# Kernel optimization log

Hardware: AMD Instinct MI355X
Metric: run time of the kernel (lower is better)

Reference implementation:

```python
import jax, jax.numpy as jnp
import numpy as np

N_NODES = 100000
N_EDGES = 1600000
D_FEAT = 128
HIDDEN = 64
N_CLASSES = 40
NEG_SLOPE = 0.01  # jax.nn.leaky_relu default, matches flax nn.leaky_relu


def glorot(key, shape):
    fan_in, fan_out = shape
    return jax.random.normal(key, shape, dtype=jnp.float32) * jnp.sqrt(2.0 / (fan_in + fan_out))


def setup_inputs() -> dict:
    key = jax.random.key(0)
    ks = jax.random.split(key, 8)
    nodes = jax.random.normal(ks[0], (N_NODES, D_FEAT), dtype=jnp.float32)
    senders = jax.random.randint(ks[1], (N_EDGES,), 0, N_NODES, dtype=jnp.int32)
    receivers = jax.random.randint(ks[2], (N_EDGES,), 0, N_NODES, dtype=jnp.int32)
    W1 = glorot(ks[3], (D_FEAT, HIDDEN))
    b1 = jnp.zeros((HIDDEN,), jnp.float32)
    W2 = glorot(ks[4], (HIDDEN, HIDDEN))
    b2 = jnp.zeros((HIDDEN,), jnp.float32)
    W3 = glorot(ks[5], (HIDDEN, N_CLASSES))
    b3 = jnp.zeros((N_CLASSES,), jnp.float32)
    return {"nodes": nodes, "senders": senders, "receivers": receivers,
            "W1": W1, "b1": b1, "W2": W2, "b2": b2, "W3": W3, "b3": b3}


def gcn_aggregate(x, senders, receivers, n_nodes):
    """jraph.GraphConvolution symmetric_normalization aggregation (post update_node_fn)."""
    ones = jnp.ones(senders.shape[0], dtype=x.dtype)
    sender_deg = jax.ops.segment_sum(ones, senders, num_segments=n_nodes)
    receiver_deg = jax.ops.segment_sum(ones, receivers, num_segments=n_nodes)
    x = x * jax.lax.rsqrt(jnp.maximum(sender_deg, 1.0))[:, None]
    x = jax.ops.segment_sum(x[senders], receivers, num_segments=n_nodes)  # [N, F]
    x = x * jax.lax.rsqrt(jnp.maximum(receiver_deg, 1.0))[:, None]
    return x


def reference(nodes, senders, receivers, W1, b1, W2, b2, W3, b3):
    n = nodes.shape[0]
    # Layer 1: GraphConvolution(MLP([hidden, hidden], leaky_relu))
    h = jax.nn.leaky_relu(nodes @ W1 + b1, NEG_SLOPE)
    h = jax.nn.leaky_relu(h @ W2 + b2, NEG_SLOPE)
    h = gcn_aggregate(h, senders, receivers, n)
    # Dropout is deterministic (training=False) -> identity
    # Layer 2: GraphConvolution(Dense(number_classes))
    h = h @ W3 + b3
    h = gcn_aggregate(h, senders, receivers, n)
    return jax.nn.softmax(h, axis=-1)
```

## Files before the change

kernel.cpp:

```cpp
#include <hip/hip_runtime.h>
#include <hip/hip_fp16.h>

#define NEG_SLOPE 0.01f
#define RANGE_BITS 15
#define RANGE (1 << RANGE_BITS)
#define HWORDS (RANGE / 2)
#define SLICE_BITS 16
#define SLICE (1 << SLICE_BITS)
#define PSTRIDE 64

typedef _Float16 f16x8 __attribute__((ext_vector_type(8)));
typedef float f32x4 __attribute__((ext_vector_type(4)));

__device__ __forceinline__ float lrelu(float x) { return x > 0.f ? x : NEG_SLOPE * x; }

__device__ __forceinline__ unsigned pack2h(float a, float b) {
    __half2 h = __floats2half2_rn(a, b);
    unsigned u; __builtin_memcpy(&u, &h, 4); return u;
}
__device__ __forceinline__ float2 unpack2(unsigned u) {
    __half2 h = *reinterpret_cast<__half2*>(&u);
    return __half22float2(h);
}
__device__ __forceinline__ f16x8 u4h8(uint4 u) {
    f16x8 r; __builtin_memcpy(&r, &u, 16); return r;
}

__global__ __launch_bounds__(1024) void count_kernel(
    const int* __restrict__ snd, const int* __restrict__ rcv,
    unsigned* __restrict__ partial, unsigned short* __restrict__ pos16,
    int nE, int NR, int NS)
{
    __shared__ unsigned hist[HWORDS];
    const int b = blockIdx.x;
    const int a = b / (NR * NS);
    const int rem = b - a * NR * NS;
    const int r = rem / NS;
    const int s = rem - r * NS;
    const int t = threadIdx.x;
    for (int k = t; k < HWORDS; k += 1024) hist[k] = 0u;
    __syncthreads();
    const int base = r << RANGE_BITS;
    const int lo = s << SLICE_BITS;
    const int hi = min(lo + SLICE, nE);
    const int n4 = (hi - lo) >> 2;
    const int* arr = (a == 0) ? rcv : snd;
    const int4* arr4 = (const int4*)(arr + lo);
    if (a == 0) {
        for (int i4 = t; i4 < n4; i4 += 1024) {
            const int4 v = arr4[i4];
            const int ib = lo + i4 * 4;
            int vv[4] = {v.x, v.y, v.z, v.w};
#pragma unroll
            for (int c = 0; c < 4; ++c) {
                const unsigned d = (unsigned)(vv[c] - base);
                if (d < (unsigned)RANGE) {
                    const unsigned sh = (d & 1u) << 4;
                    const unsigned old = atomicAdd(&hist[d >> 1], 1u << sh);
                    pos16[ib + c] = (unsigned short)((old >> sh) & 0xffffu);
                }
            }
        }
        for (int i = lo + n4 * 4 + t; i < hi; i += 1024) {
            const unsigned d = (unsigned)(arr[i] - base);
            if (d < (unsigned)RANGE) {
                const unsigned sh = (d & 1u) << 4;
                const unsigned old = atomicAdd(&hist[d >> 1], 1u << sh);
                pos16[i] = (unsigned short)((old >> sh) & 0xffffu);
            }
        }
    } else {
        for (int i4 = t; i4 < n4; i4 += 1024) {
            const int4 v = arr4[i4];
            int vv[4] = {v.x, v.y, v.z, v.w};
#pragma unroll
            for (int c = 0; c < 4; ++c) {
                const unsigned d = (unsigned)(vv[c] - base);
                if (d < (unsigned)RANGE) atomicAdd(&hist[d >> 1], 1u << ((d & 1u) << 4));
            }
        }
        for (int i = lo + n4 * 4 + t; i < hi; i += 1024) {
            const unsigned d = (unsigned)(arr[i] - base);
            if (d < (unsigned)RANGE) atomicAdd(&hist[d >> 1], 1u << ((d & 1u) << 4));
        }
    }
    __syncthreads();
    unsigned* dst = partial + (size_t)((a * NR + r) * NS + s) * HWORDS;
    for (int k = t; k < HWORDS; k += 1024) dst[k] = hist[k];
}

__global__ __launch_bounds__(256) void scanp_kernel(
    unsigned* __restrict__ partial,
    int* __restrict__ dr_i,
    float* __restrict__ rin, float* __restrict__ rout,
    int nN, int NR, int NS)
{
    const int gid = blockIdx.x * 256 + threadIdx.x;
    if (gid >= NR * HWORDS) return;
    const int r  = gid >> (RANGE_BITS - 1);
    const int wd = gid & (HWORDS - 1);
    unsigned* prcv = partial + (size_t)(r * NS) * HWORDS + wd;
    unsigned run0 = 0, run1 = 0;
    for (int s = 0; s < NS; ++s) {
        unsigned* p = prcv + (size_t)s * HWORDS;
        const unsigned c = *p;
        *p = run0 | (run1 << 16);
        run0 += c & 0xffffu;
        run1 += c >> 16;
    }
    const unsigned* psnd = partial + (size_t)((NR + r) * NS) * HWORDS + wd;
    unsigned t0 = 0, t1 = 0;
    for (int s = 0; s < NS; ++s) {
        const unsigned c = psnd[(size_t)s * HWORDS];
        t0 += c & 0xffffu;
        t1 += c >> 16;
    }
    const int n0 = (r << RANGE_BITS) + 2 * wd;
    if (n0 < nN) {
        dr_i[n0] = (int)run0;
        rout[n0] = rsqrtf(fmaxf((float)run0, 1.f));
        rin[n0]  = rsqrtf(fmaxf((float)t0, 1.f));
    }
    if (n0 + 1 < nN) {
        dr_i[n0 + 1] = (int)run1;
        rout[n0 + 1] = rsqrtf(fmaxf((float)run1, 1.f));
        rin[n0 + 1]  = rsqrtf(fmaxf((float)t1, 1.f));
    }
}

__global__ __launch_bounds__(256) void scan1_kernel(const int* __restrict__ cnt,
                                                    int* __restrict__ rowptr,
                                                    int* __restrict__ bsums, int n)
{
    __shared__ int sd[256];
    const int t = threadIdx.x;
    const int base = blockIdx.x * 1024 + t * 4;
    int v0 = (base + 0 < n) ? cnt[base + 0] : 0;
    int v1 = (base + 1 < n) ? cnt[base + 1] : 0;
    int v2 = (base + 2 < n) ? cnt[base + 2] : 0;
    int v3 = (base + 3 < n) ? cnt[base + 3] : 0;
    const int p1 = v0, p2 = v0 + v1, p3 = v0 + v1 + v2;
    const int tot = p3 + v3;
    sd[t] = tot;
    __syncthreads();
    for (int off = 1; off < 256; off <<= 1) {
        int y = (t >= off) ? sd[t - off] : 0;
        __syncthreads();
        sd[t] += y;
        __syncthreads();
    }
    const int excl = sd[t] - tot;
    if (base + 0 < n) rowptr[base + 0] = excl;
    if (base + 1 < n) rowptr[base + 1] = excl + p1;
    if (base + 2 < n) rowptr[base + 2] = excl + p2;
    if (base + 3 < n) rowptr[base + 3] = excl + p3;
    if (t == 255) bsums[blockIdx.x] = sd[255];
}

__global__ __launch_bounds__(256) void scan2_kernel(int* __restrict__ bsums, int nb)
{
    __shared__ int sd[256];
    const int t = threadIdx.x;
    const int v = (t < nb) ? bsums[t] : 0;
    sd[t] = v;
    __syncthreads();
    for (int off = 1; off < 256; off <<= 1) {
        int y = (t >= off) ? sd[t - off] : 0;
        __syncthreads();
        sd[t] += y;
        __syncthreads();
    }
    if (t < nb) bsums[t] = sd[t] - v;
}

__global__ __launch_bounds__(256) void scan3_kernel(int* __restrict__ rowptr,
                                                    const int* __restrict__ bsums,
                                                    int n, int nE)
{
    const int gid = blockIdx.x * 256 + threadIdx.x;
    if (gid < n) rowptr[gid] += bsums[gid >> 10];
    if (gid == 0) rowptr[n] = nE;
}

__global__ __launch_bounds__(256) void fillmlp_kernel(
    const float* __restrict__ X, const float* __restrict__ W1, const float* __restrict__ b1,
    const float* __restrict__ W2, const float* __restrict__ b2, const float* __restrict__ W3,
    const float* __restrict__ rin, __half* __restrict__ p, int nN, int NB_MLP,
    const int* __restrict__ snd, const int* __restrict__ rcv,
    const unsigned short* __restrict__ pos16, const unsigned* __restrict__ partial,
    const int* __restrict__ rowptr, int* __restrict__ csr_src, int nE, int NS)
{
    __shared__ uint4 R1[1024];
    __shared__ uint4 R2[512];

    const int blk = (int)blockIdx.x;
    if (blk < NB_MLP) {
        const int t    = threadIdx.x;
        const int w    = t >> 6;
        const int l    = t & 63;
        const int lrow = l & 15;
        const int lq   = l >> 4;
        const int row0 = blk * 64;

        {
            const int c = l;
            for (int ch = 0; ch < 4; ++ch) {
                const int kc = 4 * w + ch;
                const float* wp = W1 + (kc * 8) * 64 + c;
                uint4 u;
                u.x = pack2h(wp[0],       wp[64]);
                u.y = pack2h(wp[2 * 64],  wp[3 * 64]);
                u.z = pack2h(wp[4 * 64],  wp[5 * 64]);
                u.w = pack2h(wp[6 * 64],  wp[7 * 64]);
                R1[c * 16 + (kc ^ (c & 7))] = u;
            }
        }

        const int grow = row0 + 16 * w + lrow;
        const bool rowok = grow < nN;
        const float* xr = X + (size_t)grow * 128 + lq * 8;

        float4 xa[4], xb[4];
#pragma unroll
        for (int ks = 0; ks < 4; ++ks) {
            xa[ks] = make_float4(0.f, 0.f, 0.f, 0.f);
            xb[ks] = xa[ks];
            if (rowok) {
                xa[ks] = *(const float4*)(xr + 32 * ks);
                xb[ks] = *(const float4*)(xr + 32 * ks + 4);
            }
        }
        __syncthreads();

        f32x4 acc1[4];
#pragma unroll
        for (int nt = 0; nt < 4; ++nt) acc1[nt] = (f32x4){0.f, 0.f, 0.f, 0.f};

#pragma unroll
        for (int ks = 0; ks < 4; ++ks) {
            uint4 au;
            au.x = pack2h(xa[ks].x, xa[ks].y); au.y = pack2h(xa[ks].z, xa[ks].w);
            au.z = pack2h(xb[ks].x, xb[ks].y); au.w = pack2h(xb[ks].z, xb[ks].w);
            const f16x8 af = u4h8(au);
            const int kc = 4 * ks + lq;
#pragma unroll
            for (int nt = 0; nt < 4; ++nt) {
                const int c = 16 * nt + lrow;
                const uint4 bu = R1[c * 16 + (kc ^ (c & 7))];
                acc1[nt] = __builtin_amdgcn_mfma_f32_16x16x32_f16(af, u4h8(bu), acc1[nt], 0, 0, 0);
            }
        }
        __syncthreads();

        {
            __half* hh = (__half*)R2;
#pragma unroll
            for (int nt = 0; nt < 4; ++nt) {
                const int col = 16 * nt + lrow;
                const float bv = b1[col];
                const int ch = col >> 3, cl = col & 7;
#pragma unroll
                for (int r = 0; r < 4; ++r) {
                    const int rw = 16 * w + 4 * lq + r;
                    hh[rw * 64 + ((ch ^ (rw & 7)) * 8) + cl] = __float2half(lrelu(acc1[nt][r] + bv));
                }
            }
            const int c = l;
#pragma unroll
            for (int ch = 0; ch < 2; ++ch) {
                const int kc = 2 * w + ch;
                const float* wp = W2 + (kc * 8) * 64 + c;
                uint4 u;
                u.x = pack2h(wp[0],      wp[64]);
                u.y = pack2h(wp[2 * 64], wp[3 * 64]);
                u.z = pack2h(wp[4 * 64], wp[5 * 64]);
                u.w = pack2h(wp[6 * 64], wp[7 * 64]);
                R1[c * 8 + (kc ^ (c & 7))] = u;
            }
            if (c < 48) {
                const bool cv = c < 40;
#pragma unroll
                for (int ch = 0; ch < 2; ++ch) {
                    const int kc = 2 * w + ch;
                    const float* wp = W3 + (kc * 8) * 40 + c;
                    uint4 u;
                    u.x = pack2h(cv ? wp[0]      : 0.f, cv ? wp[40]     : 0.f);
                    u.y = pack2h(cv ? wp[2 * 40] : 0.f, cv ? wp[3 * 40] : 0.f);
                    u.z = pack2h(cv ? wp[4 * 40] : 0.f, cv ? wp[5 * 40] : 0.f);
                    u.w = pack2h(cv ? wp[6 * 40] : 0.f, cv ? wp[7 * 40] : 0.f);
                    R1[512 + c * 8 + (kc ^ (c & 7))] = u;
                }
            }
        }
        __syncthreads();

        f32x4 acc2[4];
#pragma unroll
        for (int nt = 0; nt < 4; ++nt) acc2[nt] = (f32x4){0.f, 0.f, 0.f, 0.f};
        {
            const int ar = 16 * w + lrow;
#pragma unroll
            for (int ks = 0; ks < 2; ++ks) {
                const int kc = 4 * ks + lq;
                const f16x8 af = u4h8(R2[ar * 8 + (kc ^ (ar & 7))]);
#pragma unroll
                for (int nt = 0; nt < 4; ++nt) {
                    const int c = 16 * nt + lrow;
                    const uint4 bu = R1[c * 8 + (kc ^ (c & 7))];
                    acc2[nt] = __builtin_amdgcn_mfma_f32_16x16x32_f16(af, u4h8(bu), acc2[nt], 0, 0, 0);
                }
            }
        }
        __syncthreads();

        {
            __half* hh = (__half*)R2;
#pragma unroll
            for (int nt = 0; nt < 4; ++nt) {
                const int col = 16 * nt + lrow;
                const float bv = b2[col];
                const int ch = col >> 3, cl = col & 7;
#pragma unroll
                for (int r = 0; r < 4; ++r) {
                    const int rw = 16 * w + 4 * lq + r;
                    hh[rw * 64 + ((ch ^ (rw & 7)) * 8) + cl] = __float2half(lrelu(acc2[nt][r] + bv));
                }
            }
        }
        __syncthreads();

        f32x4 acc3[3];
#pragma unroll
        for (int nt = 0; nt < 3; ++nt) acc3[nt] = (f32x4){0.f, 0.f, 0.f, 0.f};
        {
            const int ar = 16 * w + lrow;
#pragma unroll
            for (int ks = 0; ks < 2; ++ks) {
                const int kc = 4 * ks + lq;
                const f16x8 af = u4h8(R2[ar * 8 + (kc ^ (ar & 7))]);
#pragma unroll
                for (int nt = 0; nt < 3; ++nt) {
                    const int c = 16 * nt + lrow;
                    const uint4 bu = R1[512 + c * 8 + (kc ^ (c & 7))];
                    acc3[nt] = __builtin_amdgcn_mfma_f32_16x16x32_f16(af, u4h8(bu), acc3[nt], 0, 0, 0);
                }
            }
        }
        __syncthreads();

        {
            __half* hh = (__half*)R2;
            float rs[4];
#pragma unroll
            for (int r = 0; r < 4; ++r) {
                const int gr = row0 + 16 * w + 4 * lq + r;
                rs[r] = (gr < nN) ? rin[gr] : 0.f;
            }
#pragma unroll
            for (int nt = 0; nt < 3; ++nt) {
                const int col = 16 * nt + lrow;
                if (col < 40) {
#pragma unroll
                    for (int r = 0; r < 4; ++r) {
                        const int rw = 16 * w + 4 * lq + r;
                        hh[rw * 40 + col] = __float2half(acc3[nt][r] * rs[r]);
                    }
                }
            }
            __syncthreads();
            for (int ch = t; ch < 640; ch += 256) {
                const int row = ch / 10;
                const int c = ch - row * 10;
                const int gr = row0 + row;
                if (gr < nN) {
                    uint2 v;
                    __builtin_memcpy(&v, hh + row * 40 + c * 4, 8);
                    *(uint2*)(p + (size_t)gr * PSTRIDE + c * 4) = v;
                }
            }
        }
    } else {
        const int i = (blk - NB_MLP) * 256 + (int)threadIdx.x;
        if (i >= nE) return;
        const int rv = rcv[i];
        const int r = rv >> RANGE_BITS;
        const int s = i >> SLICE_BITS;
        const unsigned pw = partial[(size_t)(r * NS + s) * HWORDS + ((rv & (RANGE - 1)) >> 1)];
        const int pref = (int)((pw >> ((rv & 1) << 4)) & 0xffffu);
        const int pos = rowptr[rv] + pref + (int)pos16[i];
        csr_src[pos] = snd[i];
    }
}

__global__ __launch_bounds__(256) void agg1_kernel(const __half* __restrict__ p,
                                                   const int* __restrict__ csr_src,
                                                   const int* __restrict__ rowptr,
                                                   const float* __restrict__ rin,
                                                   const float* __restrict__ rout,
                                                   __half* __restrict__ qbuf,
                                                   float* __restrict__ cbuf, int nN)
{
    const int gid = blockIdx.x * 256 + threadIdx.x;
    const int node = gid >> 3;
    const int j = gid & 7;
    if (node >= nN) return;
    const int beg = rowptr[node], end = rowptr[node + 1];
    const bool isch = (j < 5);
    const bool isr  = (j == 5);
    float a[8];
#pragma unroll
    for (int k = 0; k < 8; ++k) a[k] = 0.f;
    float cs = 0.f;

    for (int e = beg; e < end; e += 16) {
        int s[16];
#pragma unroll
        for (int b = 0; b < 16; ++b) {
            const int idx = e + b;
            s[b] = csr_src[idx < end ? idx : end - 1];
        }
        if (isch) {
            uint4 u[16];
#pragma unroll
            for (int b = 0; b < 16; ++b)
                u[b] = ((const uint4*)(p + (size_t)s[b] * PSTRIDE))[j];
#pragma unroll
            for (int b = 0; b < 16; ++b) {
                if (e + b < end) {
                    float2 f;
                    f = unpack2(u[b].x); a[0] += f.x; a[1] += f.y;
                    f = unpack2(u[b].y); a[2] += f.x; a[3] += f.y;
                    f = unpack2(u[b].z); a[4] += f.x; a[5] += f.y;
                    f = unpack2(u[b].w); a[6] += f.x; a[7] += f.y;
                }
            }
        } else if (isr) {
            float rr[16];
#pragma unroll
            for (int b = 0; b < 16; ++b) rr[b] = rin[s[b]];
#pragma unroll
            for (int b = 0; b < 16; ++b)
                if (e + b < end) cs += rr[b];
        }
    }

    if (isch) {
        const float sc = rin[node] * rout[node];
        uint4 o;
        o.x = pack2h(a[0] * sc, a[1] * sc);
        o.y = pack2h(a[2] * sc, a[3] * sc);
        o.z = pack2h(a[4] * sc, a[5] * sc);
        o.w = pack2h(a[6] * sc, a[7] * sc);
        ((uint4*)(qbuf + (size_t)node * PSTRIDE))[j] = o;
    } else if (isr) {
        cbuf[node] = cs * rout[node];
    }
}

__global__ __launch_bounds__(256) void agg2_kernel(const __half* __restrict__ qbuf,
                                                   const int* __restrict__ csr_src,
                                                   const int* __restrict__ rowptr,
                                                   const float* __restrict__ rout,
                                                   const float* __restrict__ cbuf,
                                                   const float* __restrict__ b3,
                                                   float* __restrict__ out, int nN)
{
    const int gid = blockIdx.x * 256 + threadIdx.x;
    const int node = gid >> 3;
    const int j = gid & 7;
    if (node >= nN) return;
    const int beg = rowptr[node], end = rowptr[node + 1];
    const bool isch = (j < 5);
    float a[8];
#pragma unroll
    for (int k = 0; k < 8; ++k) a[k] = 0.f;

    for (int e = beg; e < end; e += 16) {
        int s[16];
#pragma unroll
        for (int b = 0; b < 16; ++b) {
            const int idx = e + b;
            s[b] = csr_src[idx < end ? idx : end - 1];
        }
        if (isch) {
            uint4 u[16];
#pragma unroll
            for (int b = 0; b < 16; ++b)
                u[b] = ((const uint4*)(qbuf + (size_t)s[b] * PSTRIDE))[j];
#pragma unroll
            for (int b = 0; b < 16; ++b) {
                if (e + b < end) {
                    float2 f;
                    f = unpack2(u[b].x); a[0] += f.x; a[1] += f.y;
                    f = unpack2(u[b].y); a[2] += f.x; a[3] += f.y;
                    f = unpack2(u[b].z); a[4] += f.x; a[5] += f.y;
                    f = unpack2(u[b].w); a[6] += f.x; a[7] += f.y;
                }
            }
        }
    }

    const float ro = rout[node];
    const float c  = cbuf[node];
    float z[8];
    float m = -1e30f, ssum = 0.f;
    if (isch) {
#pragma unroll
        for (int k = 0; k < 8; ++k) {
            z[k] = ro * a[k] + c * b3[j * 8 + k];
            m = fmaxf(m, z[k]);
        }
    }
    m = fmaxf(m, __shfl_xor(m, 1));
    m = fmaxf(m, __shfl_xor(m, 2));
    m = fmaxf(m, __shfl_xor(m, 4));
    if (isch) {
#pragma unroll
        for (int k = 0; k < 8; ++k) { z[k] = __expf(z[k] - m); ssum += z[k]; }
    }
    ssum += __shfl_xor(ssum, 1);
    ssum += __shfl_xor(ssum, 2);
    ssum += __shfl_xor(ssum, 4);
    if (isch) {
        const float inv = 1.f / ssum;
        float4* orow = (float4*)(out + (size_t)node * 40);
        orow[j * 2 + 0] = make_float4(z[0] * inv, z[1] * inv, z[2] * inv, z[3] * inv);
        orow[j * 2 + 1] = make_float4(z[4] * inv, z[5] * inv, z[6] * inv, z[7] * inv);
    }
}

extern "C" void kernel_launch(void* const* d_in, const int* in_sizes, int n_in,
                              void* d_out, int out_size, void* d_ws, size_t ws_size,
                              hipStream_t stream)
{
    const float* nodes = (const float*)d_in[0];
    const int*   snd   = (const int*)d_in[1];
    const int*   rcv   = (const int*)d_in[2];
    const float* W1    = (const float*)d_in[3];
    const float* b1    = (const float*)d_in[4];
    const float* W2    = (const float*)d_in[5];
    const float* b2    = (const float*)d_in[6];
    const float* W3    = (const float*)d_in[7];
    const float* b3    = (const float*)d_in[8];

    const int nN = in_sizes[0] / 128;
    const int nE = in_sizes[1];
    const int NR = (nN + RANGE - 1) >> RANGE_BITS;
    const int NS = (nE + SLICE - 1) >> SLICE_BITS;
    const int nb1 = (nN + 1023) / 1024;
    const int NB_MLP  = (nN + 63) / 64;
    const int NB_FILL = (nE + 255) / 256;

    size_t off = 0;
    auto alloc = [&](size_t n) { size_t r = off; off += (n + 3) & ~(size_t)3; return r; };
    int*   dr_i    = (int*)d_ws + alloc(nN);
    int*   rowptr  = (int*)d_ws + alloc(nN + 1);
    int*   bsums   = (int*)d_ws + alloc(256);
    float* rin     = (float*)d_ws + alloc(nN);
    float* rout    = (float*)d_ws + alloc(nN);
    float* cbuf    = (float*)d_ws + alloc(nN);
    int*   csr_src = (int*)d_ws + alloc(nE);
    off = (off + 31) & ~(size_t)31;
    const size_t psz = (size_t)2 * NR * NS * HWORDS;
    const size_t possz = ((size_t)nE + 1) / 2;
    size_t ubase = off;
    unsigned*       partial = (unsigned*)d_ws + ubase;
    unsigned short* pos16   = (unsigned short*)((unsigned*)d_ws + ubase + psz);
    __half* qbuf = (__half*)((unsigned*)d_ws + ubase);
    off = ubase + psz + possz;
    off = (off + 31) & ~(size_t)31;
    __half* pbuf = (__half*)((int*)d_ws + off);

    count_kernel<<<2 * NR * NS, 1024, 0, stream>>>(snd, rcv, partial, pos16, nE, NR, NS);
    scanp_kernel<<<(NR * HWORDS + 255) / 256, 256, 0, stream>>>(partial, dr_i, rin, rout, nN, NR, NS);
    scan1_kernel<<<nb1, 256, 0, stream>>>(dr_i, rowptr, bsums, nN);
    scan2_kernel<<<1, 256, 0, stream>>>(bsums, nb1);
    scan3_kernel<<<(nN + 255) / 256, 256, 0, stream>>>(rowptr, bsums, nN, nE);
    fillmlp_kernel<<<NB_MLP + NB_FILL, 256, 0, stream>>>(
        nodes, W1, b1, W2, b2, W3, rin, pbuf, nN, NB_MLP,
        snd, rcv, pos16, partial, rowptr, csr_src, nE, NS);
    agg1_kernel<<<((size_t)nN * 8 + 255) / 256, 256, 0, stream>>>(pbuf, csr_src, rowptr, rin, rout, qbuf, cbuf, nN);
    agg2_kernel<<<((size_t)nN * 8 + 255) / 256, 256, 0, stream>>>(qbuf, csr_src, rowptr, rout, cbuf, b3, (float*)d_out, nN);
}
```

Before: 152.1 us.

## Fuse node MLP into count kernel and apply sender normalization during aggregation

The dense MLP (three MFMA matmuls) moves out of the fill kernel and into the degree-count/histogram kernel as extra 1024-thread blocks, each handling four 64-row tiles. Because the MLP now runs before the sender degrees exist, the rsqrt(sender_deg) scaling moves into agg1. There each gathered row is multiplied by a per-edge rin value that lane 5 loads and shares with the other lanes through a shuffle. This overlaps the MLP with the edge histogram pass and leaves the fill kernel as pure scatter. The cost is extra multiplies per edge in agg1, and the count kernel's blocks now mix very different workloads.

```diff
diff --git a/kernel.cpp b/kernel.cpp
--- a/kernel.cpp
+++ b/kernel.cpp
@@ -26,67 +26,260 @@
     f16x8 r; __builtin_memcpy(&r, &u, 16); return r;
 }
 
-__global__ __launch_bounds__(1024) void count_kernel(
+__global__ __launch_bounds__(1024) void countmlp_kernel(
     const int* __restrict__ snd, const int* __restrict__ rcv,
     unsigned* __restrict__ partial, unsigned short* __restrict__ pos16,
-    int nE, int NR, int NS)
-{
-    __shared__ unsigned hist[HWORDS];
-    const int b = blockIdx.x;
-    const int a = b / (NR * NS);
-    const int rem = b - a * NR * NS;
-    const int r = rem / NS;
-    const int s = rem - r * NS;
-    const int t = threadIdx.x;
-    for (int k = t; k < HWORDS; k += 1024) hist[k] = 0u;
-    __syncthreads();
-    const int base = r << RANGE_BITS;
-    const int lo = s << SLICE_BITS;
-    const int hi = min(lo + SLICE, nE);
-    const int n4 = (hi - lo) >> 2;
-    const int* arr = (a == 0) ? rcv : snd;
-    const int4* arr4 = (const int4*)(arr + lo);
-    if (a == 0) {
-        for (int i4 = t; i4 < n4; i4 += 1024) {
-            const int4 v = arr4[i4];
-            const int ib = lo + i4 * 4;
-            int vv[4] = {v.x, v.y, v.z, v.w};
-#pragma unroll
-            for (int c = 0; c < 4; ++c) {
-                const unsigned d = (unsigned)(vv[c] - base);
+    int nE, int NR, int NS, int NB_CNT,
+    const float* __restrict__ X, const float* __restrict__ W1, const float* __restrict__ b1,
+    const float* __restrict__ W2, const float* __restrict__ b2, const float* __restrict__ W3,
+    __half* __restrict__ p, int nN)
+{
+    __shared__ unsigned shraw[16384];
+    const int blk = (int)blockIdx.x;
+
+    if (blk < NB_CNT) {
+        unsigned* hist = shraw;
+        const int b = blk;
+        const int a = b / (NR * NS);
+        const int rem = b - a * NR * NS;
+        const int r = rem / NS;
+        const int s = rem - r * NS;
+        const int t = threadIdx.x;
+        for (int k = t; k < HWORDS; k += 1024) hist[k] = 0u;
+        __syncthreads();
+        const int base = r << RANGE_BITS;
+        const int lo = s << SLICE_BITS;
+        const int hi = min(lo + SLICE, nE);
+        const int n4 = (hi - lo) >> 2;
+        const int* arr = (a == 0) ? rcv : snd;
+        const int4* arr4 = (const int4*)(arr + lo);
+        if (a == 0) {
+            for (int i4 = t; i4 < n4; i4 += 1024) {
+                const int4 v = arr4[i4];
+                const int ib = lo + i4 * 4;
+                int vv[4] = {v.x, v.y, v.z, v.w};
+#pragma unroll
+                for (int c = 0; c < 4; ++c) {
+                    const unsigned d = (unsigned)(vv[c] - base);
+                    if (d < (unsigned)RANGE) {
+                        const unsigned sh = (d & 1u) << 4;
+                        const unsigned old = atomicAdd(&hist[d >> 1], 1u << sh);
+                        pos16[ib + c] = (unsigned short)((old >> sh) & 0xffffu);
+                    }
+                }
+            }
+            for (int i = lo + n4 * 4 + t; i < hi; i += 1024) {
+                const unsigned d = (unsigned)(arr[i] - base);
                 if (d < (unsigned)RANGE) {
                     const unsigned sh = (d & 1u) << 4;
                     const unsigned old = atomicAdd(&hist[d >> 1], 1u << sh);
-                    pos16[ib + c] = (unsigned short)((old >> sh) & 0xffffu);
-                }
-            }
-        }
-        for (int i = lo + n4 * 4 + t; i < hi; i += 1024) {
-            const unsigned d = (unsigned)(arr[i] - base);
-            if (d < (unsigned)RANGE) {
-                const unsigned sh = (d & 1u) << 4;
-                const unsigned old = atomicAdd(&hist[d >> 1], 1u << sh);
-                pos16[i] = (unsigned short)((old >> sh) & 0xffffu);
-            }
-        }
+                    pos16[i] = (unsigned short)((old >> sh) & 0xffffu);
+                }
+            }
+        } else {
+            for (int i4 = t; i4 < n4; i4 += 1024) {
+                const int4 v = arr4[i4];
+                int vv[4] = {v.x, v.y, v.z, v.w};
+#pragma unroll
+                for (int c = 0; c < 4; ++c) {
+                    const unsigned d = (unsigned)(vv[c] - base);
+                    if (d < (unsigned)RANGE) atomicAdd(&hist[d >> 1], 1u << ((d & 1u) << 4));
+                }
+            }
+            for (int i = lo + n4 * 4 + t; i < hi; i += 1024) {
+                const unsigned d = (unsigned)(arr[i] - base);
+                if (d < (unsigned)RANGE) atomicAdd(&hist[d >> 1], 1u << ((d & 1u) << 4));
+            }
+        }
+        __syncthreads();
+        unsigned* dst = partial + (size_t)((a * NR + r) * NS + s) * HWORDS;
+        for (int k = t; k < HWORDS; k += 1024) dst[k] = hist[k];
     } else {
-        for (int i4 = t; i4 < n4; i4 += 1024) {
-            const int4 v = arr4[i4];
-            int vv[4] = {v.x, v.y, v.z, v.w};
-#pragma unroll
-            for (int c = 0; c < 4; ++c) {
-                const unsigned d = (unsigned)(vv[c] - base);
-                if (d < (unsigned)RANGE) atomicAdd(&hist[d >> 1], 1u << ((d & 1u) << 4));
-            }
-        }
-        for (int i = lo + n4 * 4 + t; i < hi; i += 1024) {
-            const unsigned d = (unsigned)(arr[i] - base);
-            if (d < (unsigned)RANGE) atomicAdd(&hist[d >> 1], 1u << ((d & 1u) << 4));
-        }
-    }
-    __syncthreads();
-    unsigned* dst = partial + (size_t)((a * NR + r) * NS + s) * HWORDS;
-    for (int k = t; k < HWORDS; k += 1024) dst[k] = hist[k];
+        uint4* R1 = (uint4*)shraw;
+        const int t10 = (int)threadIdx.x;
+        const int sub = t10 >> 8;
+        const int t   = t10 & 255;
+        const int w   = t >> 6;
+        const int l   = t & 63;
+        const int lrow = l & 15;
+        const int lq   = l >> 4;
+        const int row0 = (blk - NB_CNT) * 256 + sub * 64;
+        uint4* R2 = (uint4*)shraw + 1024 + sub * 512;
+
+        if (sub == 0) {
+            const int c = l;
+            for (int ch = 0; ch < 4; ++ch) {
+                const int kc = 4 * w + ch;
+                const float* wp = W1 + (kc * 8) * 64 + c;
+                uint4 u;
+                u.x = pack2h(wp[0],       wp[64]);
+                u.y = pack2h(wp[2 * 64],  wp[3 * 64]);
+                u.z = pack2h(wp[4 * 64],  wp[5 * 64]);
+                u.w = pack2h(wp[6 * 64],  wp[7 * 64]);
+                R1[c * 16 + (kc ^ (c & 7))] = u;
+            }
+        }
+
+        const int grow = row0 + 16 * w + lrow;
+        const bool rowok = grow < nN;
+        const float* xr = X + (size_t)grow * 128 + lq * 8;
+
+        float4 xa[4], xb[4];
+#pragma unroll
+        for (int ks = 0; ks < 4; ++ks) {
+            xa[ks] = make_float4(0.f, 0.f, 0.f, 0.f);
+            xb[ks] = xa[ks];
+            if (rowok) {
+                xa[ks] = *(const float4*)(xr + 32 * ks);
+                xb[ks] = *(const float4*)(xr + 32 * ks + 4);
+            }
+        }
+        __syncthreads();
+
+        f32x4 acc1[4];
+#pragma unroll
+        for (int nt = 0; nt < 4; ++nt) acc1[nt] = (f32x4){0.f, 0.f, 0.f, 0.f};
+
+#pragma unroll
+        for (int ks = 0; ks < 4; ++ks) {
+            uint4 au;
+            au.x = pack2h(xa[ks].x, xa[ks].y); au.y = pack2h(xa[ks].z, xa[ks].w);
+            au.z = pack2h(xb[ks].x, xb[ks].y); au.w = pack2h(xb[ks].z, xb[ks].w);
+            const f16x8 af = u4h8(au);
+            const int kc = 4 * ks + lq;
+#pragma unroll
+            for (int nt = 0; nt < 4; ++nt) {
+                const int c = 16 * nt + lrow;
+                const uint4 bu = R1[c * 16 + (kc ^ (c & 7))];
+                acc1[nt] = __builtin_amdgcn_mfma_f32_16x16x32_f16(af, u4h8(bu), acc1[nt], 0, 0, 0);
+            }
+        }
+        __syncthreads();
+
+        {
+            __half* hh = (__half*)R2;
+#pragma unroll
+            for (int nt = 0; nt < 4; ++nt) {
+                const int col = 16 * nt + lrow;
+                const float bv = b1[col];
+                const int ch = col >> 3, cl = col & 7;
+#pragma unroll
+                for (int r = 0; r < 4; ++r) {
+                    const int rw = 16 * w + 4 * lq + r;
+                    hh[rw * 64 + ((ch ^ (rw & 7)) * 8) + cl] = __float2half(lrelu(acc1[nt][r] + bv));
+                }
+            }
+            if (sub == 0) {
+                const int c = l;
+#pragma unroll
+                for (int ch = 0; ch < 2; ++ch) {
+                    const int kc = 2 * w + ch;
+                    const float* wp = W2 + (kc * 8) * 64 + c;
+                    uint4 u;
+                    u.x = pack2h(wp[0],      wp[64]);
+                    u.y = pack2h(wp[2 * 64], wp[3 * 64]);
+                    u.z = pack2h(wp[4 * 64], wp[5 * 64]);
+                    u.w = pack2h(wp[6 * 64], wp[7 * 64]);
+                    R1[c * 8 + (kc ^ (c & 7))] = u;
+                }
+                if (c < 48) {
+                    const bool cv = c < 40;
+#pragma unroll
+                    for (int ch = 0; ch < 2; ++ch) {
+                        const int kc = 2 * w + ch;
+                        const float* wp = W3 + (kc * 8) * 40 + c;
+                        uint4 u;
+                        u.x = pack2h(cv ? wp[0]      : 0.f, cv ? wp[40]     : 0.f);
+                        u.y = pack2h(cv ? wp[2 * 40] : 0.f, cv ? wp[3 * 40] : 0.f);
+                        u.z = pack2h(cv ? wp[4 * 40] : 0.f, cv ? wp[5 * 40] : 0.f);
+                        u.w = pack2h(cv ? wp[6 * 40] : 0.f, cv ? wp[7 * 40] : 0.f);
+                        R1[512 + c * 8 + (kc ^ (c & 7))] = u;
+                    }
+                }
+            }
+        }
+        __syncthreads();
+
+        f32x4 acc2[4];
+#pragma unroll
+        for (int nt = 0; nt < 4; ++nt) acc2[nt] = (f32x4){0.f, 0.f, 0.f, 0.f};
+        {
+            const int ar = 16 * w + lrow;
+#pragma unroll
+            for (int ks = 0; ks < 2; ++ks) {
+                const int kc = 4 * ks + lq;
+                const f16x8 af = u4h8(R2[ar * 8 + (kc ^ (ar & 7))]);
+#pragma unroll
+                for (int nt = 0; nt < 4; ++nt) {
+                    const int c = 16 * nt + lrow;
+                    const uint4 bu = R1[c * 8 + (kc ^ (c & 7))];
+                    acc2[nt] = __builtin_amdgcn_mfma_f32_16x16x32_f16(af, u4h8(bu), acc2[nt], 0, 0, 0);
+                }
+            }
+        }
+        __syncthreads();
+
+        {
+            __half* hh = (__half*)R2;
+#pragma unroll
+            for (int nt = 0; nt < 4; ++nt) {
+                const int col = 16 * nt + lrow;
+                const float bv = b2[col];
+                const int ch = col >> 3, cl = col & 7;
+#pragma unroll
+                for (int r = 0; r < 4; ++r) {
+                    const int rw = 16 * w + 4 * lq + r;
+                    hh[rw * 64 + ((ch ^ (rw & 7)) * 8) + cl] = __float2half(lrelu(acc2[nt][r] + bv));
+                }
+            }
+        }
+        __syncthreads();
+
+        f32x4 acc3[3];
+#pragma unroll
+        for (int nt = 0; nt < 3; ++nt) acc3[nt] = (f32x4){0.f, 0.f, 0.f, 0.f};
+        {
+            const int ar = 16 * w + lrow;
+#pragma unroll
+            for (int ks = 0; ks < 2; ++ks) {
+                const int kc = 4 * ks + lq;
+                const f16x8 af = u4h8(R2[ar * 8 + (kc ^ (ar & 7))]);
+#pragma unroll
+                for (int nt = 0; nt < 3; ++nt) {
+                    const int c = 16 * nt + lrow;
+                    const uint4 bu = R1[512 + c * 8 + (kc ^ (c & 7))];
+                    acc3[nt] = __builtin_amdgcn_mfma_f32_16x16x32_f16(af, u4h8(bu), acc3[nt], 0, 0, 0);
+                }
+            }
+        }
+        __syncthreads();
+
+        {
+            __half* hh = (__half*)R2;
+#pragma unroll
+            for (int nt = 0; nt < 3; ++nt) {
+                const int col = 16 * nt + lrow;
+                if (col < 40) {
+#pragma unroll
+                    for (int r = 0; r < 4; ++r) {
+                        const int rw = 16 * w + 4 * lq + r;
+                        hh[rw * 40 + col] = __float2half(acc3[nt][r]);
+                    }
+                }
+            }
+            __syncthreads();
+            for (int ch = t; ch < 640; ch += 256) {
+                const int row = ch / 10;
+                const int c = ch - row * 10;
+                const int gr = row0 + row;
+                if (gr < nN) {
+                    uint2 v;
+                    __builtin_memcpy(&v, hh + row * 40 + c * 4, 8);
+                    *(uint2*)(p + (size_t)gr * PSTRIDE + c * 4) = v;
+                }
+            }
+        }
+    }
 }
 
 __global__ __launch_bounds__(256) void scanp_kernel(
@@ -182,214 +375,21 @@
     if (gid == 0) rowptr[n] = nE;
 }
 
-__global__ __launch_bounds__(256) void fillmlp_kernel(
-    const float* __restrict__ X, const float* __restrict__ W1, const float* __restrict__ b1,
-    const float* __restrict__ W2, const float* __restrict__ b2, const float* __restrict__ W3,
-    const float* __restrict__ rin, __half* __restrict__ p, int nN, int NB_MLP,
+__global__ __launch_bounds__(256) void fill_kernel(
     const int* __restrict__ snd, const int* __restrict__ rcv,
     const unsigned short* __restrict__ pos16, const unsigned* __restrict__ partial,
-    const int* __restrict__ rowptr, int* __restrict__ csr_src, int nE, int NS)
-{
-    __shared__ uint4 R1[1024];
-    __shared__ uint4 R2[512];
-
-    const int blk = (int)blockIdx.x;
-    if (blk < NB_MLP) {
-        const int t    = threadIdx.x;
-        const int w    = t >> 6;
-        const int l    = t & 63;
-        const int lrow = l & 15;
-        const int lq   = l >> 4;
-        const int row0 = blk * 64;
-
-        {
-            const int c = l;
-            for (int ch = 0; ch < 4; ++ch) {
-                const int kc = 4 * w + ch;
-                const float* wp = W1 + (kc * 8) * 64 + c;
-                uint4 u;
-                u.x = pack2h(wp[0],       wp[64]);
-                u.y = pack2h(wp[2 * 64],  wp[3 * 64]);
-                u.z = pack2h(wp[4 * 64],  wp[5 * 64]);
-                u.w = pack2h(wp[6 * 64],  wp[7 * 64]);
-                R1[c * 16 + (kc ^ (c & 7))] = u;
-            }
-        }
-
-        const int grow = row0 + 16 * w + lrow;
-        const bool rowok = grow < nN;
-        const float* xr = X + (size_t)grow * 128 + lq * 8;
-
-        float4 xa[4], xb[4];
-#pragma unroll
-        for (int ks = 0; ks < 4; ++ks) {
-            xa[ks] = make_float4(0.f, 0.f, 0.f, 0.f);
-            xb[ks] = xa[ks];
-            if (rowok) {
-                xa[ks] = *(const float4*)(xr + 32 * ks);
-                xb[ks] = *(const float4*)(xr + 32 * ks + 4);
-            }
-        }
-        __syncthreads();
-
-        f32x4 acc1[4];
-#pragma unroll
-        for (int nt = 0; nt < 4; ++nt) acc1[nt] = (f32x4){0.f, 0.f, 0.f, 0.f};
-
-#pragma unroll
-        for (int ks = 0; ks < 4; ++ks) {
-            uint4 au;
-            au.x = pack2h(xa[ks].x, xa[ks].y); au.y = pack2h(xa[ks].z, xa[ks].w);
-            au.z = pack2h(xb[ks].x, xb[ks].y); au.w = pack2h(xb[ks].z, xb[ks].w);
-            const f16x8 af = u4h8(au);
-            const int kc = 4 * ks + lq;
-#pragma unroll
-            for (int nt = 0; nt < 4; ++nt) {
-                const int c = 16 * nt + lrow;
-                const uint4 bu = R1[c * 16 + (kc ^ (c & 7))];
-                acc1[nt] = __builtin_amdgcn_mfma_f32_16x16x32_f16(af, u4h8(bu), acc1[nt], 0, 0, 0);
-            }
-        }
-        __syncthreads();
-
-        {
-            __half* hh = (__half*)R2;
-#pragma unroll
-            for (int nt = 0; nt < 4; ++nt) {
-                const int col = 16 * nt + lrow;
-                const float bv = b1[col];
-                const int ch = col >> 3, cl = col & 7;
-#pragma unroll
-                for (int r = 0; r < 4; ++r) {
-                    const int rw = 16 * w + 4 * lq + r;
-                    hh[rw * 64 + ((ch ^ (rw & 7)) * 8) + cl] = __float2half(lrelu(acc1[nt][r] + bv));
-                }
-            }
-            const int c = l;
-#pragma unroll
-            for (int ch = 0; ch < 2; ++ch) {
-                const int kc = 2 * w + ch;
-                const float* wp = W2 + (kc * 8) * 64 + c;
-                uint4 u;
-                u.x = pack2h(wp[0],      wp[64]);
-                u.y = pack2h(wp[2 * 64], wp[3 * 64]);
-                u.z = pack2h(wp[4 * 64], wp[5 * 64]);
-                u.w = pack2h(wp[6 * 64], wp[7 * 64]);
-                R1[c * 8 + (kc ^ (c & 7))] = u;
-            }
-            if (c < 48) {
-                const bool cv = c < 40;
-#pragma unroll
-                for (int ch = 0; ch < 2; ++ch) {
-                    const int kc = 2 * w + ch;
-                    const float* wp = W3 + (kc * 8) * 40 + c;
-                    uint4 u;
-                    u.x = pack2h(cv ? wp[0]      : 0.f, cv ? wp[40]     : 0.f);
-                    u.y = pack2h(cv ? wp[2 * 40] : 0.f, cv ? wp[3 * 40] : 0.f);
-                    u.z = pack2h(cv ? wp[4 * 40] : 0.f, cv ? wp[5 * 40] : 0.f);
-                    u.w = pack2h(cv ? wp[6 * 40] : 0.f, cv ? wp[7 * 40] : 0.f);
-                    R1[512 + c * 8 + (kc ^ (c & 7))] = u;
-                }
-            }
-        }
-        __syncthreads();
-
-        f32x4 acc2[4];
-#pragma unroll
-        for (int nt = 0; nt < 4; ++nt) acc2[nt] = (f32x4){0.f, 0.f, 0.f, 0.f};
-        {
-            const int ar = 16 * w + lrow;
-#pragma unroll
-            for (int ks = 0; ks < 2; ++ks) {
-                const int kc = 4 * ks + lq;
-                const f16x8 af = u4h8(R2[ar * 8 + (kc ^ (ar & 7))]);
-#pragma unroll
-                for (int nt = 0; nt < 4; ++nt) {
-                    const int c = 16 * nt + lrow;
-                    const uint4 bu = R1[c * 8 + (kc ^ (c & 7))];
-                    acc2[nt] = __builtin_amdgcn_mfma_f32_16x16x32_f16(af, u4h8(bu), acc2[nt], 0, 0, 0);
-                }
-            }
-        }
-        __syncthreads();
-
-        {
-            __half* hh = (__half*)R2;
-#pragma unroll
-            for (int nt = 0; nt < 4; ++nt) {
-                const int col = 16 * nt + lrow;
-                const float bv = b2[col];
-                const int ch = col >> 3, cl = col & 7;
-#pragma unroll
-                for (int r = 0; r < 4; ++r) {
-                    const int rw = 16 * w + 4 * lq + r;
-                    hh[rw * 64 + ((ch ^ (rw & 7)) * 8) + cl] = __float2half(lrelu(acc2[nt][r] + bv));
-                }
-            }
-        }
-        __syncthreads();
-
-        f32x4 acc3[3];
-#pragma unroll
-        for (int nt = 0; nt < 3; ++nt) acc3[nt] = (f32x4){0.f, 0.f, 0.f, 0.f};
-        {
-            const int ar = 16 * w + lrow;
-#pragma unroll
-            for (int ks = 0; ks < 2; ++ks) {
-                const int kc = 4 * ks + lq;
-                const f16x8 af = u4h8(R2[ar * 8 + (kc ^ (ar & 7))]);
-#pragma unroll
-                for (int nt = 0; nt < 3; ++nt) {
-                    const int c = 16 * nt + lrow;
-                    const uint4 bu = R1[512 + c * 8 + (kc ^ (c & 7))];
-                    acc3[nt] = __builtin_amdgcn_mfma_f32_16x16x32_f16(af, u4h8(bu), acc3[nt], 0, 0, 0);
-                }
-            }
-        }
-        __syncthreads();
-
-        {
-            __half* hh = (__half*)R2;
-            float rs[4];
-#pragma unroll
-            for (int r = 0; r < 4; ++r) {
-                const int gr = row0 + 16 * w + 4 * lq + r;
-                rs[r] = (gr < nN) ? rin[gr] : 0.f;
-            }
-#pragma unroll
-            for (int nt = 0; nt < 3; ++nt) {
-                const int col = 16 * nt + lrow;
-                if (col < 40) {
-#pragma unroll
-                    for (int r = 0; r < 4; ++r) {
-                        const int rw = 16 * w + 4 * lq + r;
-                        hh[rw * 40 + col] = __float2half(acc3[nt][r] * rs[r]);
-                    }
-                }
-            }
-            __syncthreads();
-            for (int ch = t; ch < 640; ch += 256) {
-                const int row = ch / 10;
-                const int c = ch - row * 10;
-                const int gr = row0 + row;
-                if (gr < nN) {
-                    uint2 v;
-                    __builtin_memcpy(&v, hh + row * 40 + c * 4, 8);
-                    *(uint2*)(p + (size_t)gr * PSTRIDE + c * 4) = v;
-                }
-            }
-        }
-    } else {
-        const int i = (blk - NB_MLP) * 256 + (int)threadIdx.x;
-        if (i >= nE) return;
-        const int rv = rcv[i];
-        const int r = rv >> RANGE_BITS;
-        const int s = i >> SLICE_BITS;
-        const unsigned pw = partial[(size_t)(r * NS + s) * HWORDS + ((rv & (RANGE - 1)) >> 1)];
-        const int pref = (int)((pw >> ((rv & 1) << 4)) & 0xffffu);
-        const int pos = rowptr[rv] + pref + (int)pos16[i];
-        csr_src[pos] = snd[i];
-    }
+    const int* __restrict__ rowptr, int* __restrict__ csr_src,
+    int nE, int NS)
+{
+    const int i = blockIdx.x * 256 + threadIdx.x;
+    if (i >= nE) return;
+    const int rv = rcv[i];
+    const int r = rv >> RANGE_BITS;
+    const int s = i >> SLICE_BITS;
+    const unsigned pw = partial[(size_t)(r * NS + s) * HWORDS + ((rv & (RANGE - 1)) >> 1)];
+    const int pref = (int)((pw >> ((rv & 1) << 4)) & 0xffffu);
+    const int pos = rowptr[rv] + pref + (int)pos16[i];
+    csr_src[pos] = snd[i];
 }
 
 __global__ __launch_bounds__(256) void agg1_kernel(const __half* __restrict__ p,
@@ -404,6 +404,8 @@
     const int node = gid >> 3;
     const int j = gid & 7;
     if (node >= nN) return;
+    const int l = (int)(threadIdx.x & 63);
+    const int src5 = (l & ~7) | 5;
     const int beg = rowptr[node], end = rowptr[node + 1];
     const bool isch = (j < 5);
     const bool isr  = (j == 5);
@@ -419,28 +421,30 @@
             const int idx = e + b;
             s[b] = csr_src[idx < end ? idx : end - 1];
         }
+        uint4 u[16];
         if (isch) {
-            uint4 u[16];
 #pragma unroll
             for (int b = 0; b < 16; ++b)
                 u[b] = ((const uint4*)(p + (size_t)s[b] * PSTRIDE))[j];
-#pragma unroll
-            for (int b = 0; b < 16; ++b) {
-                if (e + b < end) {
+        } else if (isr) {
+#pragma unroll
+            for (int b = 0; b < 16; ++b)
+                u[b].x = __float_as_uint(rin[s[b]]);
+        }
+#pragma unroll
+        for (int b = 0; b < 16; ++b) {
+            const float rr = __shfl(__uint_as_float(u[b].x), src5);
+            if (e + b < end) {
+                if (isch) {
                     float2 f;
-                    f = unpack2(u[b].x); a[0] += f.x; a[1] += f.y;
-                    f = unpack2(u[b].y); a[2] += f.x; a[3] += f.y;
-                    f = unpack2(u[b].z); a[4] += f.x; a[5] += f.y;
-                    f = unpack2(u[b].w); a[6] += f.x; a[7] += f.y;
-                }
-            }
-        } else if (isr) {
-            float rr[16];
-#pragma unroll
-            for (int b = 0; b < 16; ++b) rr[b] = rin[s[b]];
-#pragma unroll
-            for (int b = 0; b < 16; ++b)
-                if (e + b < end) cs += rr[b];
+                    f = unpack2(u[b].x); a[0] += rr * f.x; a[1] += rr * f.y;
+                    f = unpack2(u[b].y); a[2] += rr * f.x; a[3] += rr * f.y;
+                    f = unpack2(u[b].z); a[4] += rr * f.x; a[5] += rr * f.y;
+                    f = unpack2(u[b].w); a[6] += rr * f.x; a[7] += rr * f.y;
+                } else if (isr) {
+                    cs += rr;
+                }
+            }
         }
     }
 
@@ -548,8 +552,8 @@
     const int NR = (nN + RANGE - 1) >> RANGE_BITS;
     const int NS = (nE + SLICE - 1) >> SLICE_BITS;
     const int nb1 = (nN + 1023) / 1024;
-    const int NB_MLP  = (nN + 63) / 64;
-    const int NB_FILL = (nE + 255) / 256;
+    const int NB_CNT  = 2 * NR * NS;
+    const int NB_MLP4 = (nN + 255) / 256;
 
     size_t off = 0;
     auto alloc = [&](size_t n) { size_t r = off; off += (n + 3) & ~(size_t)3; return r; };
@@ -571,14 +575,14 @@
     off = (off + 31) & ~(size_t)31;
     __half* pbuf = (__half*)((int*)d_ws + off);
 
-    count_kernel<<<2 * NR * NS, 1024, 0, stream>>>(snd, rcv, partial, pos16, nE, NR, NS);
+    countmlp_kernel<<<NB_CNT + NB_MLP4, 1024, 0, stream>>>(
+        snd, rcv, partial, pos16, nE, NR, NS, NB_CNT,
+        nodes, W1, b1, W2, b2, W3, pbuf, nN);
     scanp_kernel<<<(NR * HWORDS + 255) / 256, 256, 0, stream>>>(partial, dr_i, rin, rout, nN, NR, NS);
     scan1_kernel<<<nb1, 256, 0, stream>>>(dr_i, rowptr, bsums, nN);
     scan2_kernel<<<1, 256, 0, stream>>>(bsums, nb1);
     scan3_kernel<<<(nN + 255) / 256, 256, 0, stream>>>(rowptr, bsums, nN, nE);
-    fillmlp_kernel<<<NB_MLP + NB_FILL, 256, 0, stream>>>(
-        nodes, W1, b1, W2, b2, W3, rin, pbuf, nN, NB_MLP,
-        snd, rcv, pos16, partial, rowptr, csr_src, nE, NS);
+    fill_kernel<<<(nE + 255) / 256, 256, 0, stream>>>(snd, rcv, pos16, partial, rowptr, csr_src, nE, NS);
     agg1_kernel<<<((size_t)nN * 8 + 255) / 256, 256, 0, stream>>>(pbuf, csr_src, rowptr, rin, rout, qbuf, cbuf, nN);
     agg2_kernel<<<((size_t)nN * 8 + 255) / 256, 256, 0, stream>>>(qbuf, csr_src, rowptr, rout, cbuf, b3, (float*)d_out, nN);
 }
```

Result: slower. 156.9 us (+3.1%).
